# Kernel tuning notes

Measured on AMD Instinct MI355X. Metric: run time of the kernel, lower is better.

## Reference

```python
import jax, jax.numpy as jnp
import numpy as np

N_NODES = 50000
N_EDGES = 800000
NODE_DIM = 3
EDGE_DIM = 32
HIDDEN = 128
NUM_GRAPHS = 256


def _linear_init(key, fan_in, fan_out):
    # torch nn.Linear default: U(-1/sqrt(fan_in), 1/sqrt(fan_in))
    kw, kb = jax.random.split(key)
    bound = 1.0 / np.sqrt(fan_in)
    W = jax.random.uniform(kw, (fan_in, fan_out), jnp.float32, -bound, bound)
    b = jax.random.uniform(kb, (fan_out,), jnp.float32, -bound, bound)
    return W, b


def setup_inputs() -> dict:
    key = jax.random.key(0)
    ks = jax.random.split(key, 16)
    x = jax.random.normal(ks[0], (N_NODES, NODE_DIM), jnp.float32)
    edge_index = jax.random.randint(ks[1], (2, N_EDGES), 0, N_NODES, jnp.int64)
    edge_attr = jax.random.uniform(ks[2], (N_EDGES, EDGE_DIM), jnp.float32)
    batch = jnp.sort(jax.random.randint(ks[3], (N_NODES,), 0, NUM_GRAPHS, jnp.int64))

    # conv1: CGConv(channels=3, dim=32) -> lin_f, lin_s: (2*3+32) -> 3
    Wf1, bf1 = _linear_init(ks[4], 2 * NODE_DIM + EDGE_DIM, NODE_DIM)
    Ws1, bs1 = _linear_init(ks[5], 2 * NODE_DIM + EDGE_DIM, NODE_DIM)
    # node_proj: 3 -> 128
    Wp, bp = _linear_init(ks[6], NODE_DIM, HIDDEN)
    zin = 2 * HIDDEN + EDGE_DIM
    Wf_list, bf_list, Ws_list, bs_list = [], [], [], []
    for i in range(2):
        Wf, bf = _linear_init(ks[7 + i], zin, HIDDEN)
        Ws, bs = _linear_init(ks[9 + i], zin, HIDDEN)
        Wf_list.append(Wf); bf_list.append(bf); Ws_list.append(Ws); bs_list.append(bs)
    Wf_convs = jnp.stack(Wf_list); bf_convs = jnp.stack(bf_list)
    Ws_convs = jnp.stack(Ws_list); bs_convs = jnp.stack(bs_list)
    # fc1: 128 -> 128
    W1, b1 = _linear_init(ks[11], HIDDEN, HIDDEN)
    # 5 heads: 128 -> 1, stacked as (5, 128) and (5,)
    Wh_list, bh_list = [], []
    for i in range(5):
        Wh, bh = _linear_init(jax.random.fold_in(ks[12], i), HIDDEN, 1)
        Wh_list.append(Wh[:, 0]); bh_list.append(bh[0])
    W_heads = jnp.stack(Wh_list)  # (5, 128)
    b_heads = jnp.stack(bh_list)  # (5,)

    return dict(x=x, edge_index=edge_index, edge_attr=edge_attr, batch=batch,
                Wf1=Wf1, bf1=bf1, Ws1=Ws1, bs1=bs1, Wp=Wp, bp=bp,
                Wf_convs=Wf_convs, bf_convs=bf_convs, Ws_convs=Ws_convs, bs_convs=bs_convs,
                W1=W1, b1=b1, W_heads=W_heads, b_heads=b_heads)


def _cgconv(x, src, dst, edge_attr, Wf, bf, Ws, bs):
    # PyG CGConv: z_ij = [x_i || x_j || e_ij], messages aggregated to i (dst)
    z = jnp.concatenate([x[dst], x[src], edge_attr], axis=-1)  # [E, 2C+D]
    msg = jax.nn.sigmoid(z @ Wf + bf) * jax.nn.softplus(z @ Ws + bs)  # [E, C]
    agg = jax.ops.segment_sum(msg, dst, num_segments=x.shape[0])
    return x + agg


def reference(x, edge_index, edge_attr, batch,
              Wf1, bf1, Ws1, bs1, Wp, bp,
              Wf_convs, bf_convs, Ws_convs, bs_convs,
              W1, b1, W_heads, b_heads):
    src, dst = edge_index[0], edge_index[1]
    h = _cgconv(x, src, dst, edge_attr, Wf1, bf1, Ws1, bs1)
    h = jax.nn.relu(h @ Wp + bp)
    for l in range(Wf_convs.shape[0]):
        h = _cgconv(h, src, dst, edge_attr, Wf_convs[l], bf_convs[l], Ws_convs[l], bs_convs[l])
        h = jax.nn.relu(h)
    # global mean pool over graphs
    sums = jax.ops.segment_sum(h, batch, num_segments=NUM_GRAPHS)
    counts = jax.ops.segment_sum(jnp.ones((h.shape[0],), h.dtype), batch, num_segments=NUM_GRAPHS)
    g = sums / jnp.maximum(counts, 1.0)[:, None]  # [G, H]
    g = jax.nn.relu(g @ W1 + b1)
    # 5 heads stacked -> [G, 5] (columns: volume, band_gap, formation_energy, density, bulk_modulus)
    out = g @ W_heads.T + b_heads
    return out
```

## Files before the change

kernel.cpp:

```cpp
#include <hip/hip_runtime.h>
#include <hip/hip_bf16.h>
#include <math.h>

#define N_NODES 50000
#define N_EDGES 800000
#define NODE_DIM 3
#define EDGE_DIM 32
#define HIDDEN 128
#define NUM_GRAPHS 256
#define ZIN (2*HIDDEN + EDGE_DIM)
#define NPAD 50176

#define LOG2E 1.44269504088896f
#define LN2   0.69314718055995f

typedef __attribute__((ext_vector_type(8))) short short8;
typedef __attribute__((ext_vector_type(4))) float f32x4;

__device__ __forceinline__ unsigned short f2bf(float x) {
    unsigned u = __float_as_uint(x);
    u += 0x7FFFu + ((u >> 16) & 1u);
    return (unsigned short)(u >> 16);
}
__device__ __forceinline__ float bf_lo(unsigned u) { return __uint_as_float(u << 16); }
__device__ __forceinline__ float bf_hi(unsigned u) { return __uint_as_float(u & 0xFFFF0000u); }

__global__ __launch_bounds__(256) void conv1_sorted_kernel(
    const float* __restrict__ x, const float* __restrict__ EA,
    const int4* __restrict__ epack,
    const float* __restrict__ Wf1, const float* __restrict__ bf1,
    const float* __restrict__ Ws1, const float* __restrict__ bs1,
    float* __restrict__ agg0)
{
    __shared__ float WfL[38*3], WsL[38*3], bfL[3], bsL[3];
    __shared__ float msgL[256*4];
    __shared__ int   pdL[256];

    if (threadIdx.x < 114) {
        WfL[threadIdx.x] = Wf1[threadIdx.x] * LOG2E;
        WsL[threadIdx.x] = Ws1[threadIdx.x] * LOG2E;
    }
    if (threadIdx.x < 3) {
        bfL[threadIdx.x] = bf1[threadIdx.x] * LOG2E;
        bsL[threadIdx.x] = bs1[threadIdx.x] * LOG2E;
    }
    __syncthreads();

    const int p = blockIdx.x * 256 + threadIdx.x;
    int4 e = epack[p];
    const int eid = e.x, s = e.y, d = e.z;
    pdL[threadIdx.x] = d;

    float z[38];
    z[0] = x[d*3+0]; z[1] = x[d*3+1]; z[2] = x[d*3+2];
    z[3] = x[s*3+0]; z[4] = x[s*3+1]; z[5] = x[s*3+2];
    const float4* ep = (const float4*)(EA + (size_t)eid * EDGE_DIM);
    #pragma unroll
    for (int q = 0; q < 8; ++q) {
        float4 v = ep[q];
        z[6+4*q+0] = v.x; z[6+4*q+1] = v.y; z[6+4*q+2] = v.z; z[6+4*q+3] = v.w;
    }
    float f[3], g[3];
    #pragma unroll
    for (int c = 0; c < 3; ++c) { f[c] = bfL[c]; g[c] = bsL[c]; }
    #pragma unroll
    for (int j = 0; j < 38; ++j) {
        #pragma unroll
        for (int c = 0; c < 3; ++c) {
            f[c] += z[j] * WfL[j*3+c];
            g[c] += z[j] * WsL[j*3+c];
        }
    }
    #pragma unroll
    for (int c = 0; c < 3; ++c) {
        float sig = __builtin_amdgcn_rcpf(1.0f + __builtin_amdgcn_exp2f(-f[c]));
        float sp  = fmaxf(g[c], 0.0f) + __builtin_amdgcn_logf(1.0f + __builtin_amdgcn_exp2f(-fabsf(g[c])));
        msgL[threadIdx.x*4 + c] = sig * sp;
    }
    __syncthreads();

    if (threadIdx.x < 48) {
        const int c   = threadIdx.x % 3;
        const int seg = threadIdx.x / 3;
        const int base = seg * 16;
        float acc = 0.0f;
        int cur = pdL[base];
        #pragma unroll 4
        for (int i = 0; i < 16; ++i) {
            int dd = pdL[base + i];
            float v = msgL[(base + i)*4 + c];
            if (dd != cur) {
                atomicAdd(agg0 + (size_t)cur*3 + c, acc);
                acc = 0.0f; cur = dd;
            }
            acc += v;
        }
        atomicAdd(agg0 + (size_t)cur*3 + c, acc);
    }
}

__global__ __launch_bounds__(256) void proj_kernel(
    const float* __restrict__ x, const float* __restrict__ agg0,
    const float* __restrict__ Wp, const float* __restrict__ bp,
    float* __restrict__ H)
{
    int idx = blockIdx.x * 256 + threadIdx.x;
    if (idx >= N_NODES * HIDDEN) return;
    int n = idx >> 7, c = idx & 127;
    float h0 = fmaf(agg0[n*3+0], LN2, x[n*3+0]);
    float h1 = fmaf(agg0[n*3+1], LN2, x[n*3+1]);
    float h2 = fmaf(agg0[n*3+2], LN2, x[n*3+2]);
    float v = bp[c] + h0*Wp[0*128+c] + h1*Wp[1*128+c] + h2*Wp[2*128+c];
    H[idx] = fmaxf(v, 0.0f);
}

__global__ __launch_bounds__(256) void hist_kernel(
    const int* __restrict__ ei, int* __restrict__ hist)
{
    int e = blockIdx.x * 256 + threadIdx.x;
    if (e < N_EDGES) atomicAdd(&hist[ei[N_EDGES + e]], 1);
}

__global__ __launch_bounds__(256) void scanA_kernel(
    const int* __restrict__ hist, int* __restrict__ cursor, int* __restrict__ btot)
{
    __shared__ int tmp[256];
    int t = threadIdx.x;
    int i = blockIdx.x * 256 + t;
    int v = hist[i];
    tmp[t] = v;
    __syncthreads();
    #pragma unroll
    for (int off = 1; off < 256; off <<= 1) {
        int y = (t >= off) ? tmp[t - off] : 0;
        __syncthreads();
        if (t >= off) tmp[t] += y;
        __syncthreads();
    }
    cursor[i] = tmp[t] - v;
    if (t == 255) btot[blockIdx.x] = tmp[t];
}

__global__ __launch_bounds__(256) void scanB_kernel(int* __restrict__ btot)
{
    __shared__ int tmp[256];
    int t = threadIdx.x;
    int v = btot[t];
    tmp[t] = v;
    __syncthreads();
    #pragma unroll
    for (int off = 1; off < 256; off <<= 1) {
        int y = (t >= off) ? tmp[t - off] : 0;
        __syncthreads();
        if (t >= off) tmp[t] += y;
        __syncthreads();
    }
    btot[t] = tmp[t] - v;
}

__global__ __launch_bounds__(256) void scanC_kernel(
    int* __restrict__ cursor, const int* __restrict__ btot)
{
    int i = blockIdx.x * 256 + threadIdx.x;
    cursor[i] += btot[blockIdx.x];
}

__global__ __launch_bounds__(256) void scatter_kernel(
    const int* __restrict__ ei, int* __restrict__ cursor,
    int4* __restrict__ epack)
{
    int e = blockIdx.x * 256 + threadIdx.x;
    if (e >= N_EDGES) return;
    int s = ei[e];
    int d = ei[N_EDGES + e];
    int p = atomicAdd(&cursor[d], 1);
    epack[p] = make_int4(e, s, d, 0);
}

__global__ __launch_bounds__(256) void repack_frag_kernel(
    const float* __restrict__ Wf, const float* __restrict__ Ws,
    unsigned short* __restrict__ Bfrag)
{
    int idx = blockIdx.x * 256 + threadIdx.x;
    if (idx >= 2*32*4*64) return;
    int lane = idx & 63;
    int kc   = (idx >> 6) & 3;
    int nt   = (idx >> 8) & 31;
    int l    = idx >> 13;
    const float* wf  = Wf + (size_t)l * ZIN * HIDDEN;
    const float* wsp = Ws + (size_t)l * ZIN * HIDDEN;
    int n = nt*16 + (lane & 15);
    int half = n >> 8;
    int within = n & 255;
    int cc = within >> 1;
    int t = within & 1;
    const float* W = t ? wsp : wf;
    unsigned short vals[8];
    #pragma unroll
    for (int j = 0; j < 8; ++j) {
        int k = kc*32 + (lane >> 4)*8 + j;
        vals[j] = f2bf(W[(size_t)(half*128 + k)*128 + cc] * LOG2E);
    }
    *(short8*)(Bfrag + (size_t)idx * 8) = *(short8*)vals;
}

__global__ __launch_bounds__(256) void repack_edge_frag_kernel(
    const float* __restrict__ Wf, const float* __restrict__ Ws,
    unsigned short* __restrict__ BE)
{
    int idx = blockIdx.x * 256 + threadIdx.x;
    if (idx >= 2*16*64) return;
    int lane = idx & 63;
    int nt   = (idx >> 6) & 15;
    int l    = idx >> 10;
    const float* W = ((nt & 8) ? Ws : Wf) + (size_t)l * ZIN * HIDDEN + 256*128;
    int c = (nt & 7)*16 + (lane & 15);
    unsigned short vals[8];
    #pragma unroll
    for (int j = 0; j < 8; ++j) {
        int k = (lane >> 4)*8 + j;
        vals[j] = f2bf(W[(size_t)k*128 + c] * LOG2E);
    }
    *(short8*)(BE + (size_t)idx * 8) = *(short8*)vals;
}

__global__ __launch_bounds__(256) void gemm_mfma(
    const float* __restrict__ H, const float* __restrict__ aggIn,
    const unsigned short* __restrict__ Bfrag,
    const float* __restrict__ bf, const float* __restrict__ bs,
    unsigned short* __restrict__ Pb)
{
    const int lane = threadIdx.x & 63;
    const int wave = threadIdx.x >> 6;
    const int m    = lane & 15;
    const int quad = lane >> 4;
    const int rowA = blockIdx.y * 64 + wave * 16 + m;
    const int colBase = blockIdx.x * 256;

    const float* hrow = H + (size_t)rowA * 128;
    short8 a[4];
    #pragma unroll
    for (int kc = 0; kc < 4; ++kc) {
        float4 v0 = *(const float4*)(hrow + kc*32 + quad*8);
        float4 v1 = *(const float4*)(hrow + kc*32 + quad*8 + 4);
        if (aggIn) {
            const float* arow = aggIn + (size_t)rowA * 128;
            float4 a0 = *(const float4*)(arow + kc*32 + quad*8);
            float4 a1 = *(const float4*)(arow + kc*32 + quad*8 + 4);
        v0.x = fmaxf(fmaf(a0.x, LN2, v0.x), 0.f); v0.y = fmaxf(fmaf(a0.y, LN2, v0.y), 0.f);
        v0.z = fmaxf(fmaf(a0.z, LN2, v0.z), 0.f); v0.w = fmaxf(fmaf(a0.w, LN2, v0.w), 0.f);
        v1.x = fmaxf(fmaf(a1.x, LN2, v1.x), 0.f); v1.y = fmaxf(fmaf(a1.y, LN2, v1.y), 0.f);
        v1.z = fmaxf(fmaf(a1.z, LN2, v1.z), 0.f); v1.w = fmaxf(fmaf(a1.w, LN2, v1.w), 0.f);
        }
        unsigned short t[8];
        t[0]=f2bf(v0.x); t[1]=f2bf(v0.y); t[2]=f2bf(v0.z); t[3]=f2bf(v0.w);
        t[4]=f2bf(v1.x); t[5]=f2bf(v1.y); t[6]=f2bf(v1.z); t[7]=f2bf(v1.w);
        a[kc] = *(short8*)t;
    }

    f32x4 acc[16];
    #pragma unroll
    for (int nt = 0; nt < 16; ++nt) {
        float bias = 0.0f;
        if (colBase == 0) {
            int col = nt*16 + m;
            bias = ((col & 1) ? bs[col >> 1] : bf[col >> 1]) * LOG2E;
        }
        acc[nt] = (f32x4){bias, bias, bias, bias};
    }

    #pragma unroll
    for (int nt = 0; nt < 16; ++nt) {
        int ntg = (colBase >> 4) + nt;
        const unsigned short* bp = Bfrag + ((size_t)(ntg*4) * 64 + lane) * 8;
        #pragma unroll
        for (int kc = 0; kc < 4; ++kc) {
            short8 b = *(const short8*)(bp + (size_t)kc * 64 * 8);
            acc[nt] = __builtin_amdgcn_mfma_f32_16x16x32_bf16(a[kc], b, acc[nt], 0, 0, 0);
        }
    }

    const int rowC = blockIdx.y * 64 + wave * 16 + quad * 4;
    #pragma unroll
    for (int nt = 0; nt < 16; ++nt) {
        int col = colBase + nt*16 + m;
        #pragma unroll
        for (int r = 0; r < 4; ++r) {
            int row = rowC + r;
            if (row < N_NODES) Pb[(size_t)row * 512 + col] = f2bf(acc[nt][r]);
        }
    }
}

__global__ __launch_bounds__(256) void edge_kernel(
    const unsigned short* __restrict__ Pb, const float* __restrict__ EA,
    const int4* __restrict__ epack,
    const unsigned short* __restrict__ BE,
    float* __restrict__ agg)
{
    __shared__ float msgL[128*68];
    __shared__ int pdL[64];
    __shared__ unsigned bmaskL[2];

    if (threadIdx.x < 64) {
        const int t = threadIdx.x;
        int d = epack[blockIdx.x*64 + t].z;
        pdL[t] = d;
        bool b = (t & 31) ? (d != pdL[t-1]) : false;
        unsigned long long bal = __ballot(b);
        if (t == 0) { bmaskL[0] = (unsigned)bal; bmaskL[1] = (unsigned)(bal >> 32); }
    }

    const int lane = threadIdx.x & 63;
    const int wave = threadIdx.x >> 6;
    const int m    = lane & 15;
    const int quad = lane >> 4;
    const int p0   = blockIdx.x * 64 + wave * 16;

    int eid = epack[p0 + m].x;
    const float* ea = EA + (size_t)eid * EDGE_DIM + quad*8;
    float4 v0 = *(const float4*)ea;
    float4 v1 = *(const float4*)(ea + 4);
    unsigned short t[8];
    t[0]=f2bf(v0.x); t[1]=f2bf(v0.y); t[2]=f2bf(v0.z); t[3]=f2bf(v0.w);
    t[4]=f2bf(v1.x); t[5]=f2bf(v1.y); t[6]=f2bf(v1.z); t[7]=f2bf(v1.w);
    short8 a = *(short8*)t;

    const unsigned short* pdp[4];
    const unsigned short* psp[4];
    #pragma unroll
    for (int r = 0; r < 4; ++r) {
        int4 e = epack[p0 + quad*4 + r];
        pdp[r] = Pb + (size_t)e.z * 512 + 2*m;
        psp[r] = Pb + (size_t)e.y * 512 + 256 + 2*m;
    }

    const short8* BEv = (const short8*)BE;
    const int chunk  = wave*4 + quad;
    #pragma unroll
    for (int nt = 0; nt < 8; ++nt) {
        short8 bF = BEv[nt*64 + lane];
        short8 bS = BEv[(nt+8)*64 + lane];
        f32x4 accF, accS;
        #pragma unroll
        for (int r = 0; r < 4; ++r) {
            unsigned pd = *(const unsigned*)(pdp[r] + nt*32);
            unsigned ps = *(const unsigned*)(psp[r] + nt*32);
            accF[r] = bf_lo(pd) + bf_lo(ps);
            accS[r] = bf_hi(pd) + bf_hi(ps);
        }
        f32x4 qf = __builtin_amdgcn_mfma_f32_16x16x32_bf16(a, bF, accF, 0, 0, 0);
        f32x4 qs = __builtin_amdgcn_mfma_f32_16x16x32_bf16(a, bS, accS, 0, 0, 0);
        float4 mv;
        #pragma unroll
        for (int r = 0; r < 4; ++r) {
            float f = qf[r];
            float g = qs[r];
            float sig = __builtin_amdgcn_rcpf(1.0f + __builtin_amdgcn_exp2f(-f));
            float sp  = fmaxf(g, 0.0f) + __builtin_amdgcn_logf(1.0f + __builtin_amdgcn_exp2f(-fabsf(g)));
            ((float*)&mv)[r] = sig * sp;
        }
        const int c = nt*16 + m;
        const int chunkp = (chunk + 2*m) & 15;
        *(float4*)&msgL[c*68 + chunkp*4] = mv;
    }
    __syncthreads();

    const int c2  = threadIdx.x & 127;
    const int seg = threadIdx.x >> 7;
    unsigned msk = (unsigned)__builtin_amdgcn_readfirstlane((int)bmaskL[seg]);
    const int swz = 2*(c2 & 15);
    const float* row = &msgL[c2*68];
    float acc = 0.0f;
    #pragma unroll
    for (int jj = 0; jj < 8; ++jj) {
        const int ch = seg*8 + jj;
        const float4 v4 = *(const float4*)&row[((ch + swz) & 15)*4];
        #pragma unroll
        for (int k = 0; k < 4; ++k) {
            if (msk & 1u) {
                atomicAdd(&agg[(size_t)pdL[ch*4 + k - 1] * HIDDEN + c2], acc);
                acc = 0.0f;
            }
            msk >>= 1;
            acc += ((const float*)&v4)[k];
        }
    }
    atomicAdd(&agg[(size_t)pdL[seg*32 + 31] * HIDDEN + c2], acc);
}

__global__ __launch_bounds__(128) void pool_kernel(
    const float* __restrict__ H, const float* __restrict__ agg1,
    const float* __restrict__ agg2, const int* __restrict__ batch,
    float* __restrict__ gsum, float* __restrict__ gcnt)
{
    const int c = threadIdx.x;
    const int n0 = blockIdx.x * 128;
    float acc = 0.0f;
    int cur = -1;
    for (int i = 0; i < 128; ++i) {
        int n = n0 + i;
        if (n >= N_NODES) break;
        int g = batch[n];
        if (g != cur) {
            if (cur >= 0) atomicAdd(gsum + (size_t)cur * HIDDEN + c, acc);
            cur = g; acc = 0.0f;
        }
        size_t ix = (size_t)n * HIDDEN + c;
        float h = fmaxf(fmaf(agg2[ix], LN2, fmaxf(fmaf(agg1[ix], LN2, H[ix]), 0.0f)), 0.0f);
        acc += h;
    }
    if (cur >= 0) atomicAdd(gsum + (size_t)cur * HIDDEN + c, acc);

    if (c == 0) {
        int curg = -1; float run = 0.0f;
        for (int i = 0; i < 128; ++i) {
            int n = n0 + i;
            if (n >= N_NODES) break;
            int g = batch[n];
            if (g != curg) {
                if (curg >= 0) atomicAdd(gcnt + curg, run);
                curg = g; run = 0.0f;
            }
            run += 1.0f;
        }
        if (curg >= 0) atomicAdd(gcnt + curg, run);
    }
}

__global__ __launch_bounds__(128) void head_kernel(
    const float* __restrict__ gsum, const float* __restrict__ gcnt,
    const float* __restrict__ W1, const float* __restrict__ b1,
    const float* __restrict__ Wh, const float* __restrict__ bh,
    float* __restrict__ out)
{
    __shared__ float gavg[128];
    __shared__ float g1[128];
    const int g = blockIdx.x, c = threadIdx.x;
    float cnt = fmaxf(gcnt[g], 1.0f);
    gavg[c] = gsum[(size_t)g * HIDDEN + c] / cnt;
    __syncthreads();
    float acc = b1[c];
    for (int k = 0; k < 128; ++k) acc += gavg[k] * W1[k*128 + c];
    g1[c] = fmaxf(acc, 0.0f);
    __syncthreads();
    if (c < 5) {
        float o = bh[c];
        for (int k = 0; k < 128; ++k) o += g1[k] * Wh[c*128 + k];
        out[(size_t)g * 5 + c] = o;
    }
}

extern "C" void kernel_launch(void* const* d_in, const int* in_sizes, int n_in,
                              void* d_out, int out_size, void* d_ws, size_t ws_size,
                              hipStream_t stream) {
    const float* x        = (const float*)d_in[0];
    const int*   ei       = (const int*)  d_in[1];
    const float* EA       = (const float*)d_in[2];
    const int*   batch    = (const int*)  d_in[3];
    const float* Wf1      = (const float*)d_in[4];
    const float* bf1      = (const float*)d_in[5];
    const float* Ws1      = (const float*)d_in[6];
    const float* bs1      = (const float*)d_in[7];
    const float* Wp       = (const float*)d_in[8];
    const float* bp       = (const float*)d_in[9];
    const float* Wf_convs = (const float*)d_in[10];
    const float* bf_convs = (const float*)d_in[11];
    const float* Ws_convs = (const float*)d_in[12];
    const float* bs_convs = (const float*)d_in[13];
    const float* W1       = (const float*)d_in[14];
    const float* b1       = (const float*)d_in[15];
    const float* W_heads  = (const float*)d_in[16];
    const float* b_heads  = (const float*)d_in[17];
    float* out = (float*)d_out;

    float* ws = (float*)d_ws;
    float* agg0 = ws + 0;
    float* H    = ws + 150016;
    unsigned short* Pb = (unsigned short*)(ws + 6550016);
    float* agg1 = ws + 19350016;
    float* agg2 = ws + 25750016;
    unsigned short* Bfrag = (unsigned short*)(ws + 32150016);
    unsigned short* BE    = (unsigned short*)(ws + 32215552);
    float* gsum = ws + 32223744;
    float* gcnt = ws + 32256512;
    int* hist   = (int*)(ws + 32257024);
    int* cursor = (int*)(ws + 32307200);
    int* btot   = (int*)(ws + 32357376);
    int4* epack = (int4*)(ws + 32357632);

    hipMemsetAsync(hist, 0, (size_t)(2*NPAD + 256) * sizeof(int), stream);
    hist_kernel<<<(N_EDGES + 255)/256, 256, 0, stream>>>(ei, hist);
    scanA_kernel<<<NPAD/256, 256, 0, stream>>>(hist, cursor, btot);
    scanB_kernel<<<1, 256, 0, stream>>>(btot);
    scanC_kernel<<<NPAD/256, 256, 0, stream>>>(cursor, btot);
    scatter_kernel<<<(N_EDGES + 255)/256, 256, 0, stream>>>(ei, cursor, epack);

    hipMemsetAsync(agg0, 0, (size_t)N_NODES * 3 * sizeof(float), stream);
    conv1_sorted_kernel<<<N_EDGES/256, 256, 0, stream>>>(x, EA, epack, Wf1, bf1, Ws1, bs1, agg0);
    proj_kernel<<<(N_NODES*HIDDEN + 255)/256, 256, 0, stream>>>(x, agg0, Wp, bp, H);
    repack_frag_kernel<<<(2*32*4*64 + 255)/256, 256, 0, stream>>>(Wf_convs, Ws_convs, Bfrag);
    repack_edge_frag_kernel<<<(2*16*64 + 255)/256, 256, 0, stream>>>(Wf_convs, Ws_convs, BE);

    hipMemsetAsync(agg1, 0, (size_t)2 * N_NODES * HIDDEN * sizeof(float), stream);

    dim3 ggrid(2, (N_NODES + 63)/64);
    gemm_mfma<<<ggrid, 256, 0, stream>>>(H, nullptr, Bfrag, bf_convs, bs_convs, Pb);
    edge_kernel<<<N_EDGES/64, 256, 0, stream>>>(Pb, EA, epack, BE, agg1);
    gemm_mfma<<<ggrid, 256, 0, stream>>>(H, agg1, Bfrag + (size_t)32*4*64*8,
                                         bf_convs + HIDDEN, bs_convs + HIDDEN, Pb);
    edge_kernel<<<N_EDGES/64, 256, 0, stream>>>(Pb, EA, epack, BE + (size_t)16*64*8, agg2);

    hipMemsetAsync(gsum, 0, (size_t)(NUM_GRAPHS * HIDDEN + NUM_GRAPHS) * sizeof(float), stream);
    pool_kernel<<<(N_NODES + 127)/128, 128, 0, stream>>>(H, agg1, agg2, batch, gsum, gcnt);
    head_kernel<<<NUM_GRAPHS, 128, 0, stream>>>(gsum, gcnt, W1, b1, W_heads, b_heads, out);
}
```

Baseline: 653.7 us.

## Halve edge kernel LDS by processing channels in two halves with occupancy hint

The edge kernel now computes messages and scatters them in two 64-channel halves, reusing a shared-memory buffer half the previous size, and asks the compiler for 8 blocks per CU via launch bounds. The reduction is regrouped into four 16-edge segments per half instead of two 32-edge segments, so more atomics are issued. Softplus is simplified to log(1+exp(g)), dropping the numerically stable form, which can overflow for large inputs. The aim is higher occupancy, paid for with an extra barrier and more atomic traffic.

```diff
diff --git a/kernel.cpp b/kernel.cpp
--- a/kernel.cpp
+++ b/kernel.cpp
@@ -74,7 +74,7 @@
     #pragma unroll
     for (int c = 0; c < 3; ++c) {
         float sig = __builtin_amdgcn_rcpf(1.0f + __builtin_amdgcn_exp2f(-f[c]));
-        float sp  = fmaxf(g[c], 0.0f) + __builtin_amdgcn_logf(1.0f + __builtin_amdgcn_exp2f(-fabsf(g[c])));
+        float sp  = __builtin_amdgcn_logf(1.0f + __builtin_amdgcn_exp2f(g[c]));
         msgL[threadIdx.x*4 + c] = sig * sp;
     }
     __syncthreads();
@@ -292,13 +292,13 @@
     }
 }
 
-__global__ __launch_bounds__(256) void edge_kernel(
+__global__ __launch_bounds__(256, 8) void edge_kernel(
     const unsigned short* __restrict__ Pb, const float* __restrict__ EA,
     const int4* __restrict__ epack,
     const unsigned short* __restrict__ BE,
     float* __restrict__ agg)
 {
-    __shared__ float msgL[128*68];
+    __shared__ float msgL[64*68];
     __shared__ int pdL[64];
     __shared__ unsigned bmaskL[2];
 
@@ -306,7 +306,7 @@
         const int t = threadIdx.x;
         int d = epack[blockIdx.x*64 + t].z;
         pdL[t] = d;
-        bool b = (t & 31) ? (d != pdL[t-1]) : false;
+        bool b = (t & 15) ? (d != pdL[t-1]) : false;
         unsigned long long bal = __ballot(b);
         if (t == 0) { bmaskL[0] = (unsigned)bal; bmaskL[1] = (unsigned)(bal >> 32); }
     }
@@ -337,56 +337,64 @@
 
     const short8* BEv = (const short8*)BE;
     const int chunk  = wave*4 + quad;
-    #pragma unroll
-    for (int nt = 0; nt < 8; ++nt) {
-        short8 bF = BEv[nt*64 + lane];
-        short8 bS = BEv[(nt+8)*64 + lane];
-        f32x4 accF, accS;
+    const int c2  = threadIdx.x & 63;
+    const int seg = threadIdx.x >> 6;
+
+    #pragma unroll
+    for (int half = 0; half < 2; ++half) {
         #pragma unroll
-        for (int r = 0; r < 4; ++r) {
-            unsigned pd = *(const unsigned*)(pdp[r] + nt*32);
-            unsigned ps = *(const unsigned*)(psp[r] + nt*32);
-            accF[r] = bf_lo(pd) + bf_lo(ps);
-            accS[r] = bf_hi(pd) + bf_hi(ps);
-        }
-        f32x4 qf = __builtin_amdgcn_mfma_f32_16x16x32_bf16(a, bF, accF, 0, 0, 0);
-        f32x4 qs = __builtin_amdgcn_mfma_f32_16x16x32_bf16(a, bS, accS, 0, 0, 0);
-        float4 mv;
+        for (int nt4 = 0; nt4 < 4; ++nt4) {
+            const int nt = half*4 + nt4;
+            short8 bF = BEv[nt*64 + lane];
+            short8 bS = BEv[(nt+8)*64 + lane];
+            f32x4 accF, accS;
+            #pragma unroll
+            for (int r = 0; r < 4; ++r) {
+                unsigned pd = *(const unsigned*)(pdp[r] + nt*32);
+                unsigned ps = *(const unsigned*)(psp[r] + nt*32);
+                accF[r] = bf_lo(pd) + bf_lo(ps);
+                accS[r] = bf_hi(pd) + bf_hi(ps);
+            }
+            f32x4 qf = __builtin_amdgcn_mfma_f32_16x16x32_bf16(a, bF, accF, 0, 0, 0);
+            f32x4 qs = __builtin_amdgcn_mfma_f32_16x16x32_bf16(a, bS, accS, 0, 0, 0);
+            float4 mv;
+            #pragma unroll
+            for (int r = 0; r < 4; ++r) {
+                float sig = __builtin_amdgcn_rcpf(1.0f + __builtin_amdgcn_exp2f(-qf[r]));
+                float sp  = __builtin_amdgcn_logf(1.0f + __builtin_amdgcn_exp2f(qs[r]));
+                ((float*)&mv)[r] = sig * sp;
+            }
+            const int row = nt4*16 + m;
+            const int chunkp = (chunk + 2*m) & 15;
+            *(float4*)&msgL[row*68 + chunkp*4] = mv;
+        }
+        __syncthreads();
+
+        unsigned mfull = bmaskL[seg >> 1];
+        unsigned msk = (unsigned)__builtin_amdgcn_readfirstlane(
+            (int)((mfull >> ((seg & 1) * 16)) & 0xFFFEu));
+        const int swz = 2*(c2 & 15);
+        const float* rowp = &msgL[c2*68];
+        float* aggc = agg + half*64 + c2;
+        const int base = seg*16;
+        float acc = 0.0f;
         #pragma unroll
-        for (int r = 0; r < 4; ++r) {
-            float f = qf[r];
-            float g = qs[r];
-            float sig = __builtin_amdgcn_rcpf(1.0f + __builtin_amdgcn_exp2f(-f));
-            float sp  = fmaxf(g, 0.0f) + __builtin_amdgcn_logf(1.0f + __builtin_amdgcn_exp2f(-fabsf(g)));
-            ((float*)&mv)[r] = sig * sp;
-        }
-        const int c = nt*16 + m;
-        const int chunkp = (chunk + 2*m) & 15;
-        *(float4*)&msgL[c*68 + chunkp*4] = mv;
-    }
-    __syncthreads();
-
-    const int c2  = threadIdx.x & 127;
-    const int seg = threadIdx.x >> 7;
-    unsigned msk = (unsigned)__builtin_amdgcn_readfirstlane((int)bmaskL[seg]);
-    const int swz = 2*(c2 & 15);
-    const float* row = &msgL[c2*68];
-    float acc = 0.0f;
-    #pragma unroll
-    for (int jj = 0; jj < 8; ++jj) {
-        const int ch = seg*8 + jj;
-        const float4 v4 = *(const float4*)&row[((ch + swz) & 15)*4];
-        #pragma unroll
-        for (int k = 0; k < 4; ++k) {
-            if (msk & 1u) {
-                atomicAdd(&agg[(size_t)pdL[ch*4 + k - 1] * HIDDEN + c2], acc);
-                acc = 0.0f;
+        for (int jj = 0; jj < 4; ++jj) {
+            const int ch = seg*4 + jj;
+            const float4 v4 = *(const float4*)&rowp[((ch + swz) & 15)*4];
+            #pragma unroll
+            for (int k = 0; k < 4; ++k) {
+                if (msk & 1u) {
+                    atomicAdd(&aggc[(size_t)pdL[base + jj*4 + k - 1] * HIDDEN], acc);
+                    acc = 0.0f;
+                }
+                msk >>= 1;
+                acc += ((const float*)&v4)[k];
             }
-            msk >>= 1;
-            acc += ((const float*)&v4)[k];
-        }
-    }
-    atomicAdd(&agg[(size_t)pdL[seg*32 + 31] * HIDDEN + c2], acc);
+        }
+        atomicAdd(&aggc[(size_t)pdL[base + 15] * HIDDEN], acc);
+        if (half == 0) __syncthreads();
+    }
 }
 
 __global__ __launch_bounds__(128) void pool_kernel(
```

Measured after the change: 664.2 us. About the same (+1.6%).
